# Optimization experiments

Hardware: AMD Instinct MI355X
Metric: run time of the kernel (lower is better)

Reference implementation:

```python
import jax, jax.numpy as jnp
import numpy as np

B = 256; M = 6; H = 448; INC = 448; EMB = 32; NHEAD = 8; DFF = 2048
OBS = 20; HOR = 30
D = EMB + 4 * NHEAD + INC      # transformer d_model = 512 (requires INC == hidden_dim)
LBUF = OBS + HOR               # 50-token buffer; index 49 is written but never read
HD = D // NHEAD
FUS_IN = D + 7 + INC           # fusion layer input = 71 + 2*hidden_dim


def _ln(x, g, b):
    mu = x.mean(-1, keepdims=True)
    var = ((x - mu) ** 2).mean(-1, keepdims=True)
    return (x - mu) * jax.lax.rsqrt(var + 1e-5) * g + b


def setup_inputs() -> dict:
    key = jax.random.key(0)
    ks = jax.random.split(key, 16)
    s = jnp.float32(0.02)
    n = lambda i, shp: jax.random.normal(ks[i], shp, dtype=jnp.float32)
    return {
        "feat_in": n(0, (B, 1, INC)),
        "loc_in": n(1, (B, M, 2)),
        "obs_trajs": n(2, (OBS, B, 2)),
        "W_emb": n(3, (2, EMB)) * s, "b_emb": jnp.zeros((EMB,)),
        "W_qkv": n(4, (D, 3 * D)) * s, "b_qkv": jnp.zeros((3 * D,)),
        "W_o": n(5, (D, D)) * s, "b_o": jnp.zeros((D,)),
        "W_ff1": n(6, (D, DFF)) * s, "b_ff1": jnp.zeros((DFF,)),
        "W_ff2": n(7, (DFF, D)) * s, "b_ff2": jnp.zeros((D,)),
        "ln1_g": jnp.ones((D,)), "ln1_b": jnp.zeros((D,)),
        "ln2_g": jnp.ones((D,)), "ln2_b": jnp.zeros((D,)),
        "W_fus": n(8, (FUS_IN, H)) * s, "b_fus": jnp.zeros((H,)),
        "W_out": n(9, (H, 2)) * s, "b_out": jnp.zeros((2,)),
    }


def reference(feat_in, loc_in, obs_trajs, W_emb, b_emb, W_qkv, b_qkv, W_o, b_o,
              W_ff1, b_ff1, W_ff2, b_ff2, ln1_g, ln1_b, ln2_g, ln2_b,
              W_fus, b_fus, W_out, b_out):
    feat = feat_in[:, 0]                                     # [B, INC]
    emb_obs = jax.nn.relu(obs_trajs @ W_emb + b_emb)         # [OBS, B, EMB]
    pos0 = jnp.zeros((LBUF, B, 2), feat.dtype).at[:OBS].set(obs_trajs)
    emb0 = jnp.zeros((LBUF, B, EMB), feat.dtype).at[:OBS].set(emb_obs)
    idxs = jnp.arange(OBS, OBS + HOR)
    scale = 1.0 / jnp.sqrt(jnp.float32(HD))
    rep = NHEAD // 2

    def run_sample(goal):                                    # goal: [B, 2]
        def step(carry, frame_idx):
            pos, emb = carry
            last = pos[frame_idx - 1]                        # [B, 2]
            dist = goal - last
            tcol = jnp.zeros((B, 1), feat.dtype) + frame_idx
            # order matches torch.cat: (emb, goal, last, dist, time, feat)
            extras = jnp.concatenate([jnp.tile(goal, (1, rep)), jnp.tile(last, (1, rep)),
                                      jnp.tile(dist, (1, rep)), jnp.tile(tcol, (1, NHEAD))], -1)
            x = jnp.concatenate([emb,
                                 jnp.broadcast_to(extras, (LBUF, B, 4 * NHEAD)),
                                 jnp.broadcast_to(feat, (LBUF, B, INC))], -1)   # [LBUF, B, D]
            qkv = x @ W_qkv + b_qkv
            q, k, v = jnp.split(qkv, 3, axis=-1)
            qh = q[frame_idx - 1].reshape(B, NHEAD, HD)      # only last query needed
            kh = k.reshape(LBUF, B, NHEAD, HD)
            vh = v.reshape(LBUF, B, NHEAD, HD)
            scores = jnp.einsum('bhd,lbhd->bhl', qh, kh) * scale
            valid = jnp.arange(LBUF) < frame_idx             # tokens 0..frame_idx-1 exist
            scores = jnp.where(valid[None, None, :], scores, -1e9)
            attn = jax.nn.softmax(scores, axis=-1)
            ctx = jnp.einsum('bhl,lbhd->bhd', attn, vh).reshape(B, D)
            a = ctx @ W_o + b_o
            x_last = x[frame_idx - 1]
            h1 = _ln(x_last + a, ln1_g, ln1_b)               # post-LN encoder layer (eval, no dropout)
            ff = jax.nn.relu(h1 @ W_ff1 + b_ff1) @ W_ff2 + b_ff2
            h2 = _ln(h1 + ff, ln2_g, ln2_b)
            fus = jnp.concatenate([h2, last, goal, dist, tcol, feat], -1)       # [B, FUS_IN]
            out = (fus @ W_fus + b_fus) @ W_out + b_out                         # [B, 2]
            pos = pos.at[frame_idx].set(out)
            emb = emb.at[frame_idx].set(jax.nn.relu(out @ W_emb + b_emb))
            return (pos, emb), out
        _, ys = jax.lax.scan(step, (pos0, emb0), idxs)
        return ys                                            # [HOR, B, 2]

    ys = jax.vmap(run_sample, in_axes=1)(loc_in)             # [M, HOR, B, 2]
    return ys.transpose(2, 0, 1, 3).reshape(B, M, HOR * 2)
```

## Files before the change

### kernel.cpp

```cpp
#include <hip/hip_runtime.h>
#include <math.h>

#define B_   256
#define N_   1536
#define OBS_ 20
#define HOR_ 30

typedef __bf16 bf16;
typedef bf16  bf16x8 __attribute__((ext_vector_type(8)));
typedef float f32x4  __attribute__((ext_vector_type(4)));

__global__ __launch_bounds__(256) void gemm_k(
    const float* __restrict__ A, int lda,
    const float* __restrict__ Bw, int ldb,
    float* __restrict__ C, bf16* __restrict__ Cb, int ldc,
    int K, const float* __restrict__ colBias)
{
    __shared__ float As[16][68];
    __shared__ float Bs[16][68];
    const int tid = threadIdx.x;
    const int tx = tid & 15, ty = tid >> 4;
    const int n0 = blockIdx.y * 64, j0 = blockIdx.x * 64;
    float acc[4][4] = {};
    const int a_kk = tid & 15, a_nn0 = tid >> 4;
    const int b_jj = tid & 63, b_kk0 = tid >> 6;
    for (int k0 = 0; k0 < K; k0 += 16) {
#pragma unroll
        for (int i = 0; i < 4; i++) {
            int nn = a_nn0 + 16 * i;
            As[a_kk][nn] = (k0 + a_kk < K) ? A[(size_t)(n0 + nn) * lda + k0 + a_kk] : 0.f;
        }
#pragma unroll
        for (int i = 0; i < 4; i++) {
            int kk = b_kk0 + 4 * i;
            Bs[kk][b_jj] = (k0 + kk < K) ? Bw[(size_t)(k0 + kk) * ldb + j0 + b_jj] : 0.f;
        }
        __syncthreads();
#pragma unroll
        for (int kk = 0; kk < 16; kk++) {
            float4 av = *(const float4*)&As[kk][ty * 4];
            float4 bv = *(const float4*)&Bs[kk][tx * 4];
            float aa[4] = {av.x, av.y, av.z, av.w};
            float bb[4] = {bv.x, bv.y, bv.z, bv.w};
#pragma unroll
            for (int i = 0; i < 4; i++)
#pragma unroll
                for (int j = 0; j < 4; j++) acc[i][j] += aa[i] * bb[j];
        }
        __syncthreads();
    }
#pragma unroll
    for (int i = 0; i < 4; i++) {
        int n = n0 + ty * 4 + i;
#pragma unroll
        for (int j = 0; j < 4; j++) {
            int jj = j0 + tx * 4 + j;
            float v = acc[i][j];
            if (colBias) v += colBias[jj];
            if (C)  C[(size_t)n * ldc + jj] = v;
            if (Cb) Cb[(size_t)n * ldc + jj] = (bf16)v;
        }
    }
}

__global__ void pack_k(const float* __restrict__ srcF, const bf16* __restrict__ srcB,
                       int srcRows, int KC, int J, int lds, bf16* __restrict__ dst)
{
    int idx = blockIdx.x * 256 + threadIdx.x;
    int total = (J / 16) * KC * 64;
    if (idx >= total) return;
    int lane = idx & 63;
    int kc = (idx >> 6) % KC;
    int jg = idx / (64 * KC);
    int k0 = kc * 32 + (lane >> 4) * 8;
    int col = jg * 16 + (lane & 15);
    bf16x8 v;
#pragma unroll
    for (int i = 0; i < 8; i++) {
        int r = k0 + i;
        float x = 0.f;
        if (r < srcRows) x = srcF ? srcF[(size_t)r * lds + col] : (float)srcB[(size_t)r * lds + col];
        v[i] = (bf16)x;
    }
    *(bf16x8*)&dst[(size_t)idx * 8] = v;
}

template<int KC>
__global__ __launch_bounds__(256) void fgemm_k(
    const bf16* __restrict__ A, int lda,
    const bf16* __restrict__ Bp,
    float* __restrict__ C, bf16* __restrict__ Cb, int ldc,
    const float* __restrict__ colBias,
    const float* __restrict__ rowMat, int ldRm,
    int doRelu)
{
    const int n0 = blockIdx.y * 32;
    const int j0g = blockIdx.x * 4;
    const int tid = threadIdx.x;
    const int w = tid >> 6, lane = tid & 63;
    const int quad = lane >> 4, m15 = lane & 15;
    const int r0 = (w & 1) * 16;
    const int cg = (w >> 1) * 2;
    const bf16* Arow = &A[(size_t)(n0 + r0 + m15) * lda + quad * 8];
    const bf16* B0 = &Bp[((size_t)(j0g + cg) * KC * 64 + lane) * 8];
    const bf16* B1 = &Bp[((size_t)(j0g + cg + 1) * KC * 64 + lane) * 8];
    f32x4 acc0 = {}, acc1 = {};
#pragma unroll 8
    for (int kc = 0; kc < KC; kc++) {
        bf16x8 af = *(const bf16x8*)&Arow[kc * 32];
        bf16x8 b0 = *(const bf16x8*)&B0[(size_t)kc * 512];
        bf16x8 b1 = *(const bf16x8*)&B1[(size_t)kc * 512];
        acc0 = __builtin_amdgcn_mfma_f32_16x16x32_bf16(af, b0, acc0, 0, 0, 0);
        acc1 = __builtin_amdgcn_mfma_f32_16x16x32_bf16(af, b1, acc1, 0, 0, 0);
    }
#pragma unroll
    for (int g = 0; g < 2; g++) {
        f32x4 a = g ? acc1 : acc0;
        int j = (j0g + cg + g) * 16 + m15;
        float cb = colBias ? colBias[j] : 0.f;
#pragma unroll
        for (int r = 0; r < 4; r++) {
            int n = n0 + r0 + quad * 4 + r;
            float v = a[r] + cb;
            if (rowMat) v += rowMat[(size_t)(n / 6) * ldRm + j];
            if (doRelu) v = fmaxf(v, 0.f);
            if (C)  C[(size_t)n * ldc + j] = v;
            if (Cb) Cb[(size_t)n * ldc + j] = (bf16)v;
        }
    }
}

__global__ __launch_bounds__(256) void emb_obs_k(
    const float* __restrict__ obs, const float* __restrict__ Wemb,
    const float* __restrict__ bemb, float* __restrict__ emb_obs)
{
    int tid = blockIdx.x * 256 + threadIdx.x;
    if (tid >= OBS_ * B_ * 32) return;
    int r = tid >> 5, e = tid & 31;
    float v = obs[r * 2] * Wemb[e] + obs[r * 2 + 1] * Wemb[32 + e] + bemb[e];
    emb_obs[tid] = fmaxf(v, 0.f);
}

__global__ __launch_bounds__(256) void weff_k(
    const float* __restrict__ Wqkv, const float* __restrict__ bqkv,
    float* __restrict__ Weff)
{
    __shared__ float qrow[512];
    const int r = blockIdx.x;
    const int t = threadIdx.x;
    for (int j = t; j < 512; j += 256)
        qrow[j] = (r < 512) ? Wqkv[(size_t)r * 1536 + j] : bqkv[j];
    __syncthreads();
    const int h = t >> 5, c = t & 31;
    float acc = 0.f;
#pragma unroll 8
    for (int d = 0; d < 64; d++)
        acc += qrow[h * 64 + d] * Wqkv[(size_t)c * 1536 + 512 + h * 64 + d];
    Weff[(size_t)r * 256 + t] = acc;
}

__global__ __launch_bounds__(256) void wov_k(
    const float* __restrict__ Wqkv, const float* __restrict__ Wo,
    bf16* __restrict__ WovCat)
{
    __shared__ float vrow[64];
    const int row = blockIdx.x;
    const int h = row >> 5, c = row & 31;
    const int t = threadIdx.x;
    if (t < 64) vrow[t] = Wqkv[(size_t)c * 1536 + 1024 + h * 64 + t];
    __syncthreads();
    for (int j = t; j < 512; j += 256) {
        float acc = 0.f;
#pragma unroll 8
        for (int d = 0; d < 64; d++)
            acc += vrow[d] * Wo[(size_t)(h * 64 + d) * 512 + j];
        WovCat[(size_t)row * 512 + j] = (bf16)acc;
    }
}

__global__ __launch_bounds__(256) void attn_k(
    const float* __restrict__ qp, const float* __restrict__ emb_obs,
    const float* __restrict__ emb_gen, bf16* __restrict__ ecA1b, int t)
{
    __shared__ float qp_s[256];
    __shared__ float emb_s[50 * 33];
    __shared__ float at_s[4][64];
    const int n = blockIdx.x, b = n / 6, tid = threadIdx.x;
    qp_s[tid] = qp[(size_t)n * 256 + tid];
    for (int idx = tid; idx < t * 32; idx += 256) {
        int l = idx >> 5, c = idx & 31;
        emb_s[l * 33 + c] = (l < OBS_) ? emb_obs[((size_t)l * B_ + b) * 32 + c]
                                       : emb_gen[((size_t)(l - OBS_) * N_ + n) * 32 + c];
    }
    __syncthreads();
    const int w = tid >> 6, lane = tid & 63;
#pragma unroll
    for (int hh = 0; hh < 2; hh++) {
        const int h = w * 2 + hh;
        float sc = -1e30f;
        if (lane < t) {
            float s_ = 0.f;
#pragma unroll 8
            for (int c = 0; c < 32; c++) s_ += emb_s[lane * 33 + c] * qp_s[h * 32 + c];
            sc = s_ * 0.125f;
        }
        float mx = sc;
#pragma unroll
        for (int o = 32; o > 0; o >>= 1) mx = fmaxf(mx, __shfl_xor(mx, o, 64));
        float e = (lane < t) ? __expf(sc - mx) : 0.f;
        float sm = e;
#pragma unroll
        for (int o = 32; o > 0; o >>= 1) sm += __shfl_xor(sm, o, 64);
        at_s[w][lane] = e / sm;
        if (lane < 32) {
            float ec = 0.f;
            for (int l = 0; l < t; l++) ec += at_s[w][l] * emb_s[l * 33 + lane];
            ecA1b[(size_t)n * 288 + h * 32 + lane] = (bf16)ec;
        }
    }
}

__global__ __launch_bounds__(256) void ln1_k(
    const float* __restrict__ a, const float* __restrict__ A1f,
    const float* __restrict__ feat, const float* __restrict__ g,
    const float* __restrict__ bt, float* __restrict__ h1f, bf16* __restrict__ h1b)
{
    __shared__ float red[8];
    const int n = blockIdx.x, b = n / 6, tid = threadIdx.x;
    float r[2]; float s = 0.f, sq = 0.f;
#pragma unroll
    for (int i = 0; i < 2; i++) {
        int j = tid + i * 256;
        float x = (j < 64) ? A1f[(size_t)n * 64 + j] : feat[(size_t)b * 448 + (j - 64)];
        float v = a[(size_t)n * 512 + j] + x;
        r[i] = v; s += v; sq += v * v;
    }
#pragma unroll
    for (int o = 32; o > 0; o >>= 1) { s += __shfl_xor(s, o, 64); sq += __shfl_xor(sq, o, 64); }
    int w = tid >> 6, lane = tid & 63;
    if (lane == 0) { red[w] = s; red[4 + w] = sq; }
    __syncthreads();
    s  = red[0] + red[1] + red[2] + red[3];
    sq = red[4] + red[5] + red[6] + red[7];
    float mu = s * (1.f / 512.f);
    float var = sq * (1.f / 512.f) - mu * mu;
    float rs = rsqrtf(var + 1e-5f);
#pragma unroll
    for (int i = 0; i < 2; i++) {
        int j = tid + i * 256;
        float v = (r[i] - mu) * rs * g[j] + bt[j];
        h1f[(size_t)n * 512 + j] = v;
        h1b[(size_t)n * 512 + j] = (bf16)v;
    }
}

__global__ __launch_bounds__(256) void ln2_k(
    const float* __restrict__ h1, const float* __restrict__ ff,
    const float* __restrict__ g, const float* __restrict__ bt,
    const float* __restrict__ small5, bf16* __restrict__ h2p)
{
    __shared__ float red[8];
    const int n = blockIdx.x, tid = threadIdx.x;
    float r[2]; float s = 0.f, sq = 0.f;
#pragma unroll
    for (int i = 0; i < 2; i++) {
        int j = tid + i * 256;
        float v = h1[(size_t)n * 512 + j] + ff[(size_t)n * 512 + j];
        r[i] = v; s += v; sq += v * v;
    }
#pragma unroll
    for (int o = 32; o > 0; o >>= 1) { s += __shfl_xor(s, o, 64); sq += __shfl_xor(sq, o, 64); }
    int w = tid >> 6, lane = tid & 63;
    if (lane == 0) { red[w] = s; red[4 + w] = sq; }
    __syncthreads();
    s  = red[0] + red[1] + red[2] + red[3];
    sq = red[4] + red[5] + red[6] + red[7];
    float mu = s * (1.f / 512.f);
    float var = sq * (1.f / 512.f) - mu * mu;
    float rs = rsqrtf(var + 1e-5f);
#pragma unroll
    for (int i = 0; i < 2; i++) {
        int j = tid + i * 256;
        h2p[(size_t)n * 544 + j] = (bf16)((r[i] - mu) * rs * g[j] + bt[j]);
    }
    if (tid < 7)  h2p[(size_t)n * 544 + 512 + tid] = (bf16)small5[n * 8 + tid];
    if (tid < 25) h2p[(size_t)n * 544 + 519 + tid] = (bf16)0.f;
}

__device__ __forceinline__ void next_state(
    int n, int b, int t, float o0, float o1, float g0, float g1, float tc,
    const float* Wemb, const float* bemb, const float* Weff, const float* featqp,
    float* emb_dst, float* A1f, bf16* ecA1b, float* small5, float* qp, float* A1s)
{
    float d0 = g0 - o0, d1 = g1 - o1;
    if (t < 32) {
        float e = fmaxf(o0 * Wemb[t] + o1 * Wemb[32 + t] + bemb[t], 0.f);
        if (emb_dst) emb_dst[t] = e;
        A1s[t] = e;
    } else if (t < 64) {
        int c = t - 32;
        float v;
        if      (c < 8)  v = (c & 1) ? g1 : g0;
        else if (c < 16) v = (c & 1) ? o1 : o0;
        else if (c < 24) v = (c & 1) ? d1 : d0;
        else             v = tc;
        A1s[t] = v;
    }
    if (t < 7) {
        float v2 = (t==0)?o0:(t==1)?o1:(t==2)?g0:(t==3)?g1:(t==4)?d0:(t==5)?d1:tc;
        small5[n * 8 + t] = v2;
    }
    __syncthreads();
    if (t < 64) {
        A1f[(size_t)n * 64 + t] = A1s[t];
        if (t >= 32) ecA1b[(size_t)n * 288 + 256 + (t - 32)] = (bf16)A1s[t];
    }
    float acc = featqp[(size_t)b * 256 + t];
#pragma unroll 8
    for (int k = 0; k < 64; k++) acc += A1s[k] * Weff[k * 256 + t];
    qp[(size_t)n * 256 + t] = acc;
}

__global__ __launch_bounds__(256) void init_k(
    const float* __restrict__ obs, const float* __restrict__ emb_obs,
    const float* __restrict__ loc, const float* __restrict__ Weff,
    const float* __restrict__ featqp,
    float* __restrict__ A1f, bf16* __restrict__ ecA1b,
    float* __restrict__ small5, float* __restrict__ qp)
{
    __shared__ float A1s[64];
    const int n = blockIdx.x, b = n / 6, m = n % 6, t = threadIdx.x;
    float o0 = obs[(19 * B_ + b) * 2], o1 = obs[(19 * B_ + b) * 2 + 1];
    float g0 = loc[b * 12 + m * 2], g1 = loc[b * 12 + m * 2 + 1];
    if (t < 32) {
        A1s[t] = emb_obs[((size_t)19 * B_ + b) * 32 + t];
    } else if (t < 64) {
        int c = t - 32; float d0 = g0 - o0, d1 = g1 - o1; float tc = 20.f;
        float v;
        if      (c < 8)  v = (c & 1) ? g1 : g0;
        else if (c < 16) v = (c & 1) ? o1 : o0;
        else if (c < 24) v = (c & 1) ? d1 : d0;
        else             v = tc;
        A1s[t] = v;
    }
    if (t < 7) {
        float d0 = g0 - o0, d1 = g1 - o1; float tc = 20.f;
        float v2 = (t==0)?o0:(t==1)?o1:(t==2)?g0:(t==3)?g1:(t==4)?d0:(t==5)?d1:tc;
        small5[n * 8 + t] = v2;
    }
    __syncthreads();
    if (t < 64) {
        A1f[(size_t)n * 64 + t] = A1s[t];
        if (t >= 32) ecA1b[(size_t)n * 288 + 256 + (t - 32)] = (bf16)A1s[t];
    }
    float acc = featqp[(size_t)b * 256 + t];
#pragma unroll 8
    for (int k = 0; k < 64; k++) acc += A1s[k] * Weff[k * 256 + t];
    qp[(size_t)n * 256 + t] = acc;
}

__global__ __launch_bounds__(256) void finish_k(
    const float* __restrict__ fusv, const float* __restrict__ Wout,
    const float* __restrict__ bout, const float* __restrict__ Wemb,
    const float* __restrict__ bemb, const float* __restrict__ loc,
    const float* __restrict__ Weff, const float* __restrict__ featqp,
    float* __restrict__ dout, float* __restrict__ emb_gen,
    float* __restrict__ A1f, bf16* __restrict__ ecA1b,
    float* __restrict__ small5, float* __restrict__ qp, int s)
{
    __shared__ float red[8];
    __shared__ float osh[2];
    __shared__ float A1s[64];
    const int n = blockIdx.x, b = n / 6, m = n % 6, t = threadIdx.x;
    float f0 = fusv[(size_t)n * 448 + t];
    float p0 = f0 * Wout[t * 2];
    float p1 = f0 * Wout[t * 2 + 1];
    if (t < 192) {
        float f1 = fusv[(size_t)n * 448 + 256 + t];
        p0 += f1 * Wout[(256 + t) * 2];
        p1 += f1 * Wout[(256 + t) * 2 + 1];
    }
#pragma unroll
    for (int o = 32; o > 0; o >>= 1) { p0 += __shfl_xor(p0, o, 64); p1 += __shfl_xor(p1, o, 64); }
    int w = t >> 6, lane = t & 63;
    if (lane == 0) { red[w] = p0; red[4 + w] = p1; }
    __syncthreads();
    if (t == 0) {
        float o0 = red[0] + red[1] + red[2] + red[3] + bout[0];
        float o1 = red[4] + red[5] + red[6] + red[7] + bout[1];
        osh[0] = o0; osh[1] = o1;
        dout[(size_t)b * 360 + m * 60 + s * 2]     = o0;
        dout[(size_t)b * 360 + m * 60 + s * 2 + 1] = o1;
    }
    __syncthreads();
    float o0 = osh[0], o1 = osh[1];
    float g0 = loc[b * 12 + m * 2], g1 = loc[b * 12 + m * 2 + 1];
    next_state(n, b, t, o0, o1, g0, g1, (float)(OBS_ + s + 1),
               Wemb, bemb, Weff, featqp,
               &emb_gen[((size_t)s * N_ + n) * 32], A1f, ecA1b, small5, qp, A1s);
}

extern "C" void kernel_launch(void* const* d_in, const int* in_sizes, int n_in,
                              void* d_out_, int out_size, void* d_ws, size_t ws_size,
                              hipStream_t stream) {
    (void)in_sizes; (void)n_in; (void)out_size; (void)ws_size;
    const float* feat  = (const float*)d_in[0];
    const float* loc   = (const float*)d_in[1];
    const float* obs   = (const float*)d_in[2];
    const float* W_emb = (const float*)d_in[3];
    const float* b_emb = (const float*)d_in[4];
    const float* W_qkv = (const float*)d_in[5];
    const float* b_qkv = (const float*)d_in[6];
    const float* W_o   = (const float*)d_in[7];
    const float* b_o   = (const float*)d_in[8];
    const float* W_ff1 = (const float*)d_in[9];
    const float* b_ff1 = (const float*)d_in[10];
    const float* W_ff2 = (const float*)d_in[11];
    const float* b_ff2 = (const float*)d_in[12];
    const float* ln1_g = (const float*)d_in[13];
    const float* ln1_b = (const float*)d_in[14];
    const float* ln2_g = (const float*)d_in[15];
    const float* ln2_b = (const float*)d_in[16];
    const float* W_fus = (const float*)d_in[17];
    const float* b_fus = (const float*)d_in[18];
    const float* W_out = (const float*)d_in[19];
    const float* b_out = (const float*)d_in[20];
    float* dout = (float*)d_out_;

    float* ws = (float*)d_ws;
    float* Weff     = ws; ws += 513 * 256;
    float* featqp   = ws; ws += 256 * 256;
    float* featv    = ws; ws += 256 * 512;
    float* featvO   = ws; ws += 256 * 512;
    float* feat_fus = ws; ws += 256 * 448;
    float* emb_obs  = ws; ws += OBS_ * B_ * 32;
    float* emb_gen  = ws; ws += HOR_ * N_ * 32;
    float* qp       = ws; ws += (size_t)N_ * 256;
    float* A1f      = ws; ws += (size_t)N_ * 64;
    float* small5   = ws; ws += (size_t)N_ * 8;
    float* h1f      = ws; ws += (size_t)N_ * 512;
    float* aF       = ws; ws += (size_t)N_ * 512;
    float* ffB      = ws; ws += (size_t)N_ * 512;
    float* fusv     = ws; ws += (size_t)N_ * 448;
    bf16* WovCat = (bf16*)ws; ws += (320 * 512) / 2;
    bf16* BpA    = (bf16*)ws; ws += (32 * 9 * 512) / 2;
    bf16* BpF1   = (bf16*)ws; ws += (128 * 16 * 512) / 2;
    bf16* BpF2   = (bf16*)ws; ws += (32 * 64 * 512) / 2;
    bf16* BpFus  = (bf16*)ws; ws += (28 * 17 * 512) / 2;
    bf16* ecA1b  = (bf16*)ws; ws += ((size_t)N_ * 288) / 2;
    bf16* h1b    = (bf16*)ws; ws += ((size_t)N_ * 512) / 2;
    bf16* f1b    = (bf16*)ws; ws += ((size_t)N_ * 2048) / 2;
    bf16* h2p    = (bf16*)ws; ws += ((size_t)N_ * 544) / 2;

    emb_obs_k<<<dim3(640), dim3(256), 0, stream>>>(obs, W_emb, b_emb, emb_obs);
    weff_k<<<dim3(513), dim3(256), 0, stream>>>(W_qkv, b_qkv, Weff);
    gemm_k<<<dim3(4, 4), dim3(256), 0, stream>>>(feat, 448, Weff + 64 * 256, 256,
        featqp, nullptr, 256, 448, Weff + 512 * 256);
    wov_k<<<dim3(256), dim3(256), 0, stream>>>(W_qkv, W_o, WovCat);
    gemm_k<<<dim3(8, 4), dim3(256), 0, stream>>>(feat, 448, W_qkv + 64 * 1536 + 1024, 1536,
        featv, nullptr, 512, 448, b_qkv + 1024);
    gemm_k<<<dim3(8, 4), dim3(256), 0, stream>>>(featv, 512, W_o, 512,
        featvO, nullptr, 512, 512, b_o);
    gemm_k<<<dim3(8, 1), dim3(256), 0, stream>>>(W_qkv + 32 * 1536 + 1024, 1536, W_o, 512,
        featv, WovCat + 256 * 512, 512, 512, nullptr);
    gemm_k<<<dim3(7, 4), dim3(256), 0, stream>>>(feat, 448, W_fus + 519 * 448, 448,
        feat_fus, nullptr, 448, 448, b_fus);
    pack_k<<<dim3(72),  dim3(256), 0, stream>>>(nullptr, WovCat, 288, 9,  512,  512,  BpA);
    pack_k<<<dim3(512), dim3(256), 0, stream>>>(W_ff1, nullptr, 512, 16, 2048, 2048, BpF1);
    pack_k<<<dim3(512), dim3(256), 0, stream>>>(W_ff2, nullptr, 2048, 64, 512, 512,  BpF2);
    pack_k<<<dim3(120), dim3(256), 0, stream>>>(W_fus, nullptr, 519, 17, 448,  448,  BpFus);
    init_k<<<dim3(N_), dim3(256), 0, stream>>>(obs, emb_obs, loc, Weff, featqp,
        A1f, ecA1b, small5, qp);

    for (int s = 0; s < HOR_; s++) {
        attn_k<<<dim3(N_), dim3(256), 0, stream>>>(qp, emb_obs, emb_gen, ecA1b, OBS_ + s);
        fgemm_k<9><<<dim3(8, 48), dim3(256), 0, stream>>>(ecA1b, 288, BpA,
            aF, nullptr, 512, nullptr, featvO, 512, 0);
        ln1_k<<<dim3(N_), dim3(256), 0, stream>>>(aF, A1f, feat, ln1_g, ln1_b, h1f, h1b);
        fgemm_k<16><<<dim3(32, 48), dim3(256), 0, stream>>>(h1b, 512, BpF1,
            nullptr, f1b, 2048, b_ff1, nullptr, 0, 1);
        fgemm_k<64><<<dim3(8, 48), dim3(256), 0, stream>>>(f1b, 2048, BpF2,
            ffB, nullptr, 512, b_ff2, nullptr, 0, 0);
        ln2_k<<<dim3(N_), dim3(256), 0, stream>>>(h1f, ffB, ln2_g, ln2_b, small5, h2p);
        fgemm_k<17><<<dim3(7, 48), dim3(256), 0, stream>>>(h2p, 544, BpFus,
            fusv, nullptr, 448, nullptr, feat_fus, 448, 0);
        finish_k<<<dim3(N_), dim3(256), 0, stream>>>(fusv, W_out, b_out, W_emb, b_emb,
            loc, Weff, featqp, dout, emb_gen, A1f, ecA1b, small5, qp, s);
    }
}
```

Before: 2.936 ms.

## Fuse attention-output GEMM with LN1, and LN2+fusion GEMM+finish into one kernel

Per step, the Wov GEMM and LayerNorm1 are merged into one MFMA kernel that computes 16-row tiles over the full 512 columns and normalises in registers. LayerNorm2, the fusion GEMM, the output projection and the next-state/query update are merged into a second kernel that keeps h2 in shared memory. A transposed Weff copy is added so the query update can use vectorised loads. This cuts the per-step loop from 8 launches to 5 and removes the aF, fusv and h2p round trips through global memory. The cost is only 96 blocks per fused kernel, which may underfill the GPU's compute units.

```diff
diff --git a/kernel.cpp b/kernel.cpp
--- a/kernel.cpp
+++ b/kernel.cpp
@@ -143,7 +143,7 @@
 
 __global__ __launch_bounds__(256) void weff_k(
     const float* __restrict__ Wqkv, const float* __restrict__ bqkv,
-    float* __restrict__ Weff)
+    float* __restrict__ Weff, float* __restrict__ WeffT)
 {
     __shared__ float qrow[512];
     const int r = blockIdx.x;
@@ -157,6 +157,7 @@
     for (int d = 0; d < 64; d++)
         acc += qrow[h * 64 + d] * Wqkv[(size_t)c * 1536 + 512 + h * 64 + d];
     Weff[(size_t)r * 256 + t] = acc;
+    if (r < 64) WeffT[(size_t)t * 64 + r] = acc;
 }
 
 __global__ __launch_bounds__(256) void wov_k(
@@ -220,105 +221,243 @@
     }
 }
 
-__global__ __launch_bounds__(256) void ln1_k(
-    const float* __restrict__ a, const float* __restrict__ A1f,
-    const float* __restrict__ feat, const float* __restrict__ g,
-    const float* __restrict__ bt, float* __restrict__ h1f, bf16* __restrict__ h1b)
-{
-    __shared__ float red[8];
-    const int n = blockIdx.x, b = n / 6, tid = threadIdx.x;
-    float r[2]; float s = 0.f, sq = 0.f;
-#pragma unroll
-    for (int i = 0; i < 2; i++) {
-        int j = tid + i * 256;
-        float x = (j < 64) ? A1f[(size_t)n * 64 + j] : feat[(size_t)b * 448 + (j - 64)];
-        float v = a[(size_t)n * 512 + j] + x;
-        r[i] = v; s += v; sq += v * v;
-    }
-#pragma unroll
-    for (int o = 32; o > 0; o >>= 1) { s += __shfl_xor(s, o, 64); sq += __shfl_xor(sq, o, 64); }
-    int w = tid >> 6, lane = tid & 63;
-    if (lane == 0) { red[w] = s; red[4 + w] = sq; }
-    __syncthreads();
-    s  = red[0] + red[1] + red[2] + red[3];
-    sq = red[4] + red[5] + red[6] + red[7];
-    float mu = s * (1.f / 512.f);
-    float var = sq * (1.f / 512.f) - mu * mu;
-    float rs = rsqrtf(var + 1e-5f);
-#pragma unroll
-    for (int i = 0; i < 2; i++) {
-        int j = tid + i * 256;
-        float v = (r[i] - mu) * rs * g[j] + bt[j];
-        h1f[(size_t)n * 512 + j] = v;
-        h1b[(size_t)n * 512 + j] = (bf16)v;
-    }
-}
-
-__global__ __launch_bounds__(256) void ln2_k(
-    const float* __restrict__ h1, const float* __restrict__ ff,
+__global__ __launch_bounds__(512) void aln1_k(
+    const bf16* __restrict__ A,
+    const bf16* __restrict__ Bp,
+    const float* __restrict__ featvO,
+    const float* __restrict__ A1f,
+    const float* __restrict__ feat,
     const float* __restrict__ g, const float* __restrict__ bt,
-    const float* __restrict__ small5, bf16* __restrict__ h2p)
-{
-    __shared__ float red[8];
-    const int n = blockIdx.x, tid = threadIdx.x;
-    float r[2]; float s = 0.f, sq = 0.f;
-#pragma unroll
-    for (int i = 0; i < 2; i++) {
-        int j = tid + i * 256;
-        float v = h1[(size_t)n * 512 + j] + ff[(size_t)n * 512 + j];
-        r[i] = v; s += v; sq += v * v;
-    }
-#pragma unroll
-    for (int o = 32; o > 0; o >>= 1) { s += __shfl_xor(s, o, 64); sq += __shfl_xor(sq, o, 64); }
-    int w = tid >> 6, lane = tid & 63;
-    if (lane == 0) { red[w] = s; red[4 + w] = sq; }
-    __syncthreads();
-    s  = red[0] + red[1] + red[2] + red[3];
-    sq = red[4] + red[5] + red[6] + red[7];
-    float mu = s * (1.f / 512.f);
-    float var = sq * (1.f / 512.f) - mu * mu;
-    float rs = rsqrtf(var + 1e-5f);
-#pragma unroll
-    for (int i = 0; i < 2; i++) {
-        int j = tid + i * 256;
-        h2p[(size_t)n * 544 + j] = (bf16)((r[i] - mu) * rs * g[j] + bt[j]);
-    }
-    if (tid < 7)  h2p[(size_t)n * 544 + 512 + tid] = (bf16)small5[n * 8 + tid];
-    if (tid < 25) h2p[(size_t)n * 544 + 519 + tid] = (bf16)0.f;
-}
-
-__device__ __forceinline__ void next_state(
-    int n, int b, int t, float o0, float o1, float g0, float g1, float tc,
-    const float* Wemb, const float* bemb, const float* Weff, const float* featqp,
-    float* emb_dst, float* A1f, bf16* ecA1b, float* small5, float* qp, float* A1s)
-{
-    float d0 = g0 - o0, d1 = g1 - o1;
-    if (t < 32) {
-        float e = fmaxf(o0 * Wemb[t] + o1 * Wemb[32 + t] + bemb[t], 0.f);
-        if (emb_dst) emb_dst[t] = e;
-        A1s[t] = e;
-    } else if (t < 64) {
-        int c = t - 32;
-        float v;
-        if      (c < 8)  v = (c & 1) ? g1 : g0;
-        else if (c < 16) v = (c & 1) ? o1 : o0;
-        else if (c < 24) v = (c & 1) ? d1 : d0;
-        else             v = tc;
-        A1s[t] = v;
-    }
-    if (t < 7) {
-        float v2 = (t==0)?o0:(t==1)?o1:(t==2)?g0:(t==3)?g1:(t==4)?d0:(t==5)?d1:tc;
-        small5[n * 8 + t] = v2;
-    }
-    __syncthreads();
-    if (t < 64) {
-        A1f[(size_t)n * 64 + t] = A1s[t];
-        if (t >= 32) ecA1b[(size_t)n * 288 + 256 + (t - 32)] = (bf16)A1s[t];
-    }
-    float acc = featqp[(size_t)b * 256 + t];
-#pragma unroll 8
-    for (int k = 0; k < 64; k++) acc += A1s[k] * Weff[k * 256 + t];
-    qp[(size_t)n * 256 + t] = acc;
+    float* __restrict__ h1f, bf16* __restrict__ h1b)
+{
+    __shared__ float redS[8][16];
+    __shared__ float redQ[8][16];
+    const int n0 = blockIdx.x * 16;
+    const int tid = threadIdx.x;
+    const int w = tid >> 6, lane = tid & 63;
+    const int quad = lane >> 4, m15 = lane & 15;
+    const bf16* Arow = &A[(size_t)(n0 + m15) * 288 + quad * 8];
+    const bf16* Bb = &Bp[((size_t)(w * 4) * 9 * 64 + lane) * 8];
+    f32x4 acc[4] = {};
+#pragma unroll 3
+    for (int kc = 0; kc < 9; kc++) {
+        bf16x8 af = *(const bf16x8*)&Arow[kc * 32];
+#pragma unroll
+        for (int gi = 0; gi < 4; gi++) {
+            bf16x8 bg = *(const bf16x8*)&Bb[(size_t)gi * 9 * 64 * 8 + (size_t)kc * 512];
+            acc[gi] = __builtin_amdgcn_mfma_f32_16x16x32_bf16(af, bg, acc[gi], 0, 0, 0);
+        }
+    }
+    float vv[4][4];
+    float sS[4] = {}, sQ[4] = {};
+#pragma unroll
+    for (int gi = 0; gi < 4; gi++) {
+        int j = (w * 4 + gi) * 16 + m15;
+#pragma unroll
+        for (int r = 0; r < 4; r++) {
+            int n = n0 + quad * 4 + r;
+            int b = n / 6;
+            float x = (j < 64) ? A1f[(size_t)n * 64 + j] : feat[(size_t)b * 448 + (j - 64)];
+            float v = acc[gi][r] + featvO[(size_t)b * 512 + j] + x;
+            vv[gi][r] = v; sS[r] += v; sQ[r] += v * v;
+        }
+    }
+#pragma unroll
+    for (int o = 1; o < 16; o <<= 1) {
+#pragma unroll
+        for (int r = 0; r < 4; r++) { sS[r] += __shfl_xor(sS[r], o, 64); sQ[r] += __shfl_xor(sQ[r], o, 64); }
+    }
+    if (m15 == 0) {
+#pragma unroll
+        for (int r = 0; r < 4; r++) { redS[w][quad * 4 + r] = sS[r]; redQ[w][quad * 4 + r] = sQ[r]; }
+    }
+    __syncthreads();
+    float mu[4], rs[4];
+#pragma unroll
+    for (int r = 0; r < 4; r++) {
+        int row = quad * 4 + r;
+        float s = 0.f, q = 0.f;
+#pragma unroll
+        for (int ww = 0; ww < 8; ww++) { s += redS[ww][row]; q += redQ[ww][row]; }
+        mu[r] = s * (1.f / 512.f);
+        float var = q * (1.f / 512.f) - mu[r] * mu[r];
+        rs[r] = rsqrtf(var + 1e-5f);
+    }
+#pragma unroll
+    for (int gi = 0; gi < 4; gi++) {
+        int j = (w * 4 + gi) * 16 + m15;
+        float gj = g[j], bj = bt[j];
+#pragma unroll
+        for (int r = 0; r < 4; r++) {
+            int n = n0 + quad * 4 + r;
+            float vn = (vv[gi][r] - mu[r]) * rs[r] * gj + bj;
+            h1f[(size_t)n * 512 + j] = vn;
+            h1b[(size_t)n * 512 + j] = (bf16)vn;
+        }
+    }
+}
+
+__global__ __launch_bounds__(256) void fusfin_k(
+    const float* __restrict__ h1f, const float* __restrict__ ffB,
+    const float* __restrict__ g2, const float* __restrict__ bt2,
+    float* __restrict__ small5,
+    const bf16* __restrict__ Bp,
+    const float* __restrict__ feat_fus,
+    const float* __restrict__ Wout, const float* __restrict__ bout,
+    const float* __restrict__ Wemb, const float* __restrict__ bemb,
+    const float* __restrict__ loc,
+    const float* __restrict__ WeffT,
+    const float* __restrict__ featqp,
+    float* __restrict__ dout, float* __restrict__ emb_gen,
+    float* __restrict__ A1f, bf16* __restrict__ ecA1b,
+    float* __restrict__ qp, int s)
+{
+    __shared__ __attribute__((aligned(16))) bf16 h2s[16][552];
+    __shared__ float red0[4][16], red1[4][16];
+    __shared__ float osh[16][2];
+    __shared__ __attribute__((aligned(16))) float A1s[16][64];
+    const int n0 = blockIdx.x * 16;
+    const int tid = threadIdx.x;
+
+    {
+        const int row = tid >> 4, li = tid & 15;
+        const int n = n0 + row;
+        float v32[32];
+        float s_ = 0.f, sq = 0.f;
+        const float* h1p = &h1f[(size_t)n * 512 + li * 32];
+        const float* ffp = &ffB[(size_t)n * 512 + li * 32];
+#pragma unroll
+        for (int i4 = 0; i4 < 8; i4++) {
+            float4 a4 = *(const float4*)&h1p[i4 * 4];
+            float4 b4 = *(const float4*)&ffp[i4 * 4];
+            float x0 = a4.x + b4.x, x1 = a4.y + b4.y, x2 = a4.z + b4.z, x3 = a4.w + b4.w;
+            v32[i4 * 4 + 0] = x0; v32[i4 * 4 + 1] = x1; v32[i4 * 4 + 2] = x2; v32[i4 * 4 + 3] = x3;
+            s_ += x0 + x1 + x2 + x3;
+            sq += x0 * x0 + x1 * x1 + x2 * x2 + x3 * x3;
+        }
+#pragma unroll
+        for (int o = 1; o < 16; o <<= 1) { s_ += __shfl_xor(s_, o, 64); sq += __shfl_xor(sq, o, 64); }
+        float mu = s_ * (1.f / 512.f);
+        float var = sq * (1.f / 512.f) - mu * mu;
+        float rs = rsqrtf(var + 1e-5f);
+#pragma unroll
+        for (int i = 0; i < 32; i++) {
+            int c = li * 32 + i;
+            float vn = (v32[i] - mu) * rs * g2[c] + bt2[c];
+            h2s[row][c] = (bf16)vn;
+        }
+        if (li == 0) {
+#pragma unroll
+            for (int sl = 0; sl < 32; sl++) {
+                float vt = (sl < 7) ? small5[(size_t)n * 8 + sl] : 0.f;
+                h2s[row][512 + sl] = (bf16)vt;
+            }
+        }
+    }
+    __syncthreads();
+
+    const int w = tid >> 6, lane = tid & 63;
+    const int quad = lane >> 4, m15 = lane & 15;
+    {
+        const bf16* Bb = &Bp[((size_t)(w * 7) * 17 * 64 + lane) * 8];
+        f32x4 acc[7] = {};
+#pragma unroll 2
+        for (int kc = 0; kc < 17; kc++) {
+            bf16x8 af = *(const bf16x8*)&h2s[m15][kc * 32 + quad * 8];
+#pragma unroll
+            for (int gi = 0; gi < 7; gi++) {
+                bf16x8 bg = *(const bf16x8*)&Bb[(size_t)gi * 17 * 64 * 8 + (size_t)kc * 512];
+                acc[gi] = __builtin_amdgcn_mfma_f32_16x16x32_bf16(af, bg, acc[gi], 0, 0, 0);
+            }
+        }
+        float p0[4] = {}, p1[4] = {};
+#pragma unroll
+        for (int gi = 0; gi < 7; gi++) {
+            int j = (w * 7 + gi) * 16 + m15;
+            float w0 = Wout[j * 2], w1 = Wout[j * 2 + 1];
+#pragma unroll
+            for (int r = 0; r < 4; r++) {
+                int n = n0 + quad * 4 + r;
+                int b = n / 6;
+                float v = acc[gi][r] + feat_fus[(size_t)b * 448 + j];
+                p0[r] += v * w0; p1[r] += v * w1;
+            }
+        }
+#pragma unroll
+        for (int o = 1; o < 16; o <<= 1) {
+#pragma unroll
+            for (int r = 0; r < 4; r++) { p0[r] += __shfl_xor(p0[r], o, 64); p1[r] += __shfl_xor(p1[r], o, 64); }
+        }
+        if (m15 == 0) {
+#pragma unroll
+            for (int r = 0; r < 4; r++) { red0[w][quad * 4 + r] = p0[r]; red1[w][quad * 4 + r] = p1[r]; }
+        }
+    }
+    __syncthreads();
+
+    if (tid < 16) {
+        const int row = tid;
+        const int n = n0 + row, b = n / 6, m = n - b * 6;
+        float o0 = red0[0][row] + red0[1][row] + red0[2][row] + red0[3][row] + bout[0];
+        float o1 = red1[0][row] + red1[1][row] + red1[2][row] + red1[3][row] + bout[1];
+        osh[row][0] = o0; osh[row][1] = o1;
+        dout[(size_t)b * 360 + m * 60 + s * 2]     = o0;
+        dout[(size_t)b * 360 + m * 60 + s * 2 + 1] = o1;
+    }
+    __syncthreads();
+
+    {
+        const int row = tid >> 4, li = tid & 15;
+        const int n = n0 + row, b = n / 6, m = n - b * 6;
+        float o0 = osh[row][0], o1 = osh[row][1];
+        float g0 = loc[b * 12 + m * 2], g1 = loc[b * 12 + m * 2 + 1];
+        float d0 = g0 - o0, d1 = g1 - o1;
+        float tc = (float)(OBS_ + s + 1);
+#pragma unroll
+        for (int ii = 0; ii < 4; ii++) {
+            int idx = li * 4 + ii;
+            float val;
+            if (idx < 32) {
+                val = fmaxf(o0 * Wemb[idx] + o1 * Wemb[32 + idx] + bemb[idx], 0.f);
+                emb_gen[((size_t)s * N_ + n) * 32 + idx] = val;
+            } else {
+                int c = idx - 32;
+                val = (c < 8)  ? ((c & 1) ? g1 : g0)
+                    : (c < 16) ? ((c & 1) ? o1 : o0)
+                    : (c < 24) ? ((c & 1) ? d1 : d0)
+                               : tc;
+                ecA1b[(size_t)n * 288 + 256 + c] = (bf16)val;
+            }
+            A1s[row][idx] = val;
+            A1f[(size_t)n * 64 + idx] = val;
+        }
+        if (li < 7) {
+            float v2 = (li == 0) ? o0 : (li == 1) ? o1 : (li == 2) ? g0 : (li == 3) ? g1
+                     : (li == 4) ? d0 : (li == 5) ? d1 : tc;
+            small5[(size_t)n * 8 + li] = v2;
+        }
+    }
+    __syncthreads();
+
+    {
+        const int c = tid;
+        float accq[16];
+#pragma unroll
+        for (int r = 0; r < 16; r++) accq[r] = featqp[(size_t)((n0 + r) / 6) * 256 + c];
+#pragma unroll 4
+        for (int k4 = 0; k4 < 16; k4++) {
+            float4 wv = *(const float4*)&WeffT[(size_t)c * 64 + k4 * 4];
+#pragma unroll
+            for (int r = 0; r < 16; r++) {
+                float4 av = *(const float4*)&A1s[r][k4 * 4];
+                float a = accq[r];
+                a += av.x * wv.x; a += av.y * wv.y; a += av.z * wv.z; a += av.w * wv.w;
+                accq[r] = a;
+            }
+        }
+#pragma unroll
+        for (int r = 0; r < 16; r++) qp[(size_t)(n0 + r) * 256 + c] = accq[r];
+    }
 }
 
 __global__ __launch_bounds__(256) void init_k(
@@ -357,47 +496,6 @@
 #pragma unroll 8
     for (int k = 0; k < 64; k++) acc += A1s[k] * Weff[k * 256 + t];
     qp[(size_t)n * 256 + t] = acc;
-}
-
-__global__ __launch_bounds__(256) void finish_k(
-    const float* __restrict__ fusv, const float* __restrict__ Wout,
-    const float* __restrict__ bout, const float* __restrict__ Wemb,
-    const float* __restrict__ bemb, const float* __restrict__ loc,
-    const float* __restrict__ Weff, const float* __restrict__ featqp,
-    float* __restrict__ dout, float* __restrict__ emb_gen,
-    float* __restrict__ A1f, bf16* __restrict__ ecA1b,
-    float* __restrict__ small5, float* __restrict__ qp, int s)
-{
-    __shared__ float red[8];
-    __shared__ float osh[2];
-    __shared__ float A1s[64];
-    const int n = blockIdx.x, b = n / 6, m = n % 6, t = threadIdx.x;
-    float f0 = fusv[(size_t)n * 448 + t];
-    float p0 = f0 * Wout[t * 2];
-    float p1 = f0 * Wout[t * 2 + 1];
-    if (t < 192) {
-        float f1 = fusv[(size_t)n * 448 + 256 + t];
-        p0 += f1 * Wout[(256 + t) * 2];
-        p1 += f1 * Wout[(256 + t) * 2 + 1];
-    }
-#pragma unroll
-    for (int o = 32; o > 0; o >>= 1) { p0 += __shfl_xor(p0, o, 64); p1 += __shfl_xor(p1, o, 64); }
-    int w = t >> 6, lane = t & 63;
-    if (lane == 0) { red[w] = p0; red[4 + w] = p1; }
-    __syncthreads();
-    if (t == 0) {
-        float o0 = red[0] + red[1] + red[2] + red[3] + bout[0];
-        float o1 = red[4] + red[5] + red[6] + red[7] + bout[1];
-        osh[0] = o0; osh[1] = o1;
-        dout[(size_t)b * 360 + m * 60 + s * 2]     = o0;
-        dout[(size_t)b * 360 + m * 60 + s * 2 + 1] = o1;
-    }
-    __syncthreads();
-    float o0 = osh[0], o1 = osh[1];
-    float g0 = loc[b * 12 + m * 2], g1 = loc[b * 12 + m * 2 + 1];
-    next_state(n, b, t, o0, o1, g0, g1, (float)(OBS_ + s + 1),
-               Wemb, bemb, Weff, featqp,
-               &emb_gen[((size_t)s * N_ + n) * 32], A1f, ecA1b, small5, qp, A1s);
 }
 
 extern "C" void kernel_launch(void* const* d_in, const int* in_sizes, int n_in,
@@ -429,6 +527,7 @@
 
     float* ws = (float*)d_ws;
     float* Weff     = ws; ws += 513 * 256;
+    float* WeffT    = ws; ws += 256 * 64;
     float* featqp   = ws; ws += 256 * 256;
     float* featv    = ws; ws += 256 * 512;
     float* featvO   = ws; ws += 256 * 512;
@@ -439,9 +538,7 @@
     float* A1f      = ws; ws += (size_t)N_ * 64;
     float* small5   = ws; ws += (size_t)N_ * 8;
     float* h1f      = ws; ws += (size_t)N_ * 512;
-    float* aF       = ws; ws += (size_t)N_ * 512;
     float* ffB      = ws; ws += (size_t)N_ * 512;
-    float* fusv     = ws; ws += (size_t)N_ * 448;
     bf16* WovCat = (bf16*)ws; ws += (320 * 512) / 2;
     bf16* BpA    = (bf16*)ws; ws += (32 * 9 * 512) / 2;
     bf16* BpF1   = (bf16*)ws; ws += (128 * 16 * 512) / 2;
@@ -450,10 +547,9 @@
     bf16* ecA1b  = (bf16*)ws; ws += ((size_t)N_ * 288) / 2;
     bf16* h1b    = (bf16*)ws; ws += ((size_t)N_ * 512) / 2;
     bf16* f1b    = (bf16*)ws; ws += ((size_t)N_ * 2048) / 2;
-    bf16* h2p    = (bf16*)ws; ws += ((size_t)N_ * 544) / 2;
 
     emb_obs_k<<<dim3(640), dim3(256), 0, stream>>>(obs, W_emb, b_emb, emb_obs);
-    weff_k<<<dim3(513), dim3(256), 0, stream>>>(W_qkv, b_qkv, Weff);
+    weff_k<<<dim3(513), dim3(256), 0, stream>>>(W_qkv, b_qkv, Weff, WeffT);
     gemm_k<<<dim3(4, 4), dim3(256), 0, stream>>>(feat, 448, Weff + 64 * 256, 256,
         featqp, nullptr, 256, 448, Weff + 512 * 256);
     wov_k<<<dim3(256), dim3(256), 0, stream>>>(W_qkv, W_o, WovCat);
@@ -474,17 +570,14 @@
 
     for (int s = 0; s < HOR_; s++) {
         attn_k<<<dim3(N_), dim3(256), 0, stream>>>(qp, emb_obs, emb_gen, ecA1b, OBS_ + s);
-        fgemm_k<9><<<dim3(8, 48), dim3(256), 0, stream>>>(ecA1b, 288, BpA,
-            aF, nullptr, 512, nullptr, featvO, 512, 0);
-        ln1_k<<<dim3(N_), dim3(256), 0, stream>>>(aF, A1f, feat, ln1_g, ln1_b, h1f, h1b);
+        aln1_k<<<dim3(N_ / 16), dim3(512), 0, stream>>>(ecA1b, BpA, featvO, A1f, feat,
+            ln1_g, ln1_b, h1f, h1b);
         fgemm_k<16><<<dim3(32, 48), dim3(256), 0, stream>>>(h1b, 512, BpF1,
             nullptr, f1b, 2048, b_ff1, nullptr, 0, 1);
         fgemm_k<64><<<dim3(8, 48), dim3(256), 0, stream>>>(f1b, 2048, BpF2,
             ffB, nullptr, 512, b_ff2, nullptr, 0, 0);
-        ln2_k<<<dim3(N_), dim3(256), 0, stream>>>(h1f, ffB, ln2_g, ln2_b, small5, h2p);
-        fgemm_k<17><<<dim3(7, 48), dim3(256), 0, stream>>>(h2p, 544, BpFus,
-            fusv, nullptr, 448, nullptr, feat_fus, 448, 0);
-        finish_k<<<dim3(N_), dim3(256), 0, stream>>>(fusv, W_out, b_out, W_emb, b_emb,
-            loc, Weff, featqp, dout, emb_gen, A1f, ecA1b, small5, qp, s);
-    }
-}
+        fusfin_k<<<dim3(N_ / 16), dim3(256), 0, stream>>>(h1f, ffB, ln2_g, ln2_b, small5,
+            BpFus, feat_fus, W_out, b_out, W_emb, b_emb, loc, WeffT, featqp,
+            dout, emb_gen, A1f, ecA1b, qp, s);
+    }
+}
```

After: 3.042 ms. +3.6%, slower.
